# Optimization experiments

Hardware: AMD Instinct MI355X
Metric: run time of the kernel (lower is better)

Reference implementation:

```python
import jax, jax.numpy as jnp
import numpy as np

N = 50000   # nodes
E = 800000  # edges
G = 256     # graphs in batch
NF, EF, H, L = 16, 8, 128, 4
EPS = 1e-5


def setup_inputs() -> dict:
    key = jax.random.key(0)
    ks = jax.random.split(key, 20)
    s = 0.05
    return {
        "x": jax.random.normal(ks[0], (N, NF), jnp.float32),
        "edge_index": jax.random.randint(ks[1], (2, E), 0, N, dtype=jnp.int32),
        "edge_attr": jax.random.uniform(ks[2], (E, EF), jnp.float32),
        "batch": jnp.sort(jax.random.randint(ks[3], (N,), 0, G, dtype=jnp.int32)),
        "W_emb": jax.random.normal(ks[4], (NF, H), jnp.float32) * s,
        "b_emb": jnp.zeros((H,), jnp.float32),
        "Wf": jax.random.normal(ks[5], (L, 2 * H + EF, H), jnp.float32) * s,
        "bf": jnp.zeros((L, H), jnp.float32),
        "Ws": jax.random.normal(ks[6], (L, 2 * H + EF, H), jnp.float32) * s,
        "bs": jnp.zeros((L, H), jnp.float32),
        "gamma": jnp.ones((L, H), jnp.float32),
        "beta": jnp.zeros((L, H), jnp.float32),
        "W1": jax.random.normal(ks[7], (H, 64), jnp.float32) * s,
        "b1": jnp.zeros((64,), jnp.float32),
        "W2": jax.random.normal(ks[8], (64, 32), jnp.float32) * s,
        "b2": jnp.zeros((32,), jnp.float32),
        "W_out": jax.random.normal(ks[9], (32, 1), jnp.float32) * s,
        "b_out": jnp.zeros((1,), jnp.float32),
    }


def reference(x, edge_index, edge_attr, batch, W_emb, b_emb, Wf, bf, Ws, bs,
              gamma, beta, W1, b1, W2, b2, W_out, b_out):
    src, dst = edge_index[0], edge_index[1]  # message j->i: x_j=h[src], x_i=h[dst]
    h = jax.nn.relu(x @ W_emb + b_emb)       # [N, H]
    for l in range(L):
        # CGConv: z_ij = [x_i, x_j, e_ij]; gated message; sum-aggregate; +x residual
        z = jnp.concatenate([h[dst], h[src], edge_attr], axis=-1)  # [E, 2H+EF]
        m = jax.nn.sigmoid(z @ Wf[l] + bf[l]) * jax.nn.softplus(z @ Ws[l] + bs[l])
        agg = jax.ops.segment_sum(m, dst, num_segments=N)
        x_new = agg + h
        # BatchNorm1d (training-mode batch statistics, biased var)
        mu = x_new.mean(axis=0)
        var = x_new.var(axis=0)
        x_new = gamma[l] * (x_new - mu) * jax.lax.rsqrt(var + EPS) + beta[l]
        x_new = jax.nn.relu(x_new)
        h = h + x_new
    # global mean pool over graphs
    cnt = jax.ops.segment_sum(jnp.ones((N,), h.dtype), batch, num_segments=G)
    pooled = jax.ops.segment_sum(h, batch, num_segments=G) / jnp.maximum(cnt, 1.0)[:, None]
    g = jax.nn.relu(pooled @ W1 + b1)
    g = jax.nn.relu(g @ W2 + b2)
    return (g @ W_out + b_out).squeeze(-1)  # [G]
```

## Files before the change

### kernel.cpp

```cpp
#include <hip/hip_runtime.h>
#include <hip/hip_bf16.h>

#define H 128
#define EFD 8
#define NLAYER 4
#define ZDIM (2*H+EFD)

typedef float f32x2 __attribute__((ext_vector_type(2)));
typedef float f32x4 __attribute__((ext_vector_type(4)));
typedef short s16x8 __attribute__((ext_vector_type(8)));
typedef _Float16 f16x4 __attribute__((ext_vector_type(4)));

#define PKFMA_LO(acc, a, b) asm("v_pk_fma_f32 %0, %1, %2, %0 op_sel:[0,0,0] op_sel_hi:[0,1,1]" : "+v"(acc) : "v"(a), "v"(b))
#define PKFMA_HI(acc, a, b) asm("v_pk_fma_f32 %0, %1, %2, %0 op_sel:[1,0,0] op_sel_hi:[1,1,1]" : "+v"(acc) : "v"(a), "v"(b))
#define PKFMA_LO_INIT(dst, a, b, c) asm("v_pk_fma_f32 %0, %1, %2, %3 op_sel:[0,0,0] op_sel_hi:[0,1,1]" : "=v"(dst) : "v"(a), "v"(b), "v"(c))

#define L2E 1.44269504088896340736f
#define LN2 0.69314718055994530942f

__device__ __forceinline__ unsigned short f2bf(float x){
    unsigned u = __float_as_uint(x);
    return (unsigned short)((u + 0x7FFFu + ((u>>16)&1u)) >> 16);
}

__global__ void embed_kernel(const float* __restrict__ x, const float* __restrict__ We,
                             const float* __restrict__ be, float* __restrict__ h, int N){
    int idx = blockIdx.x*blockDim.x + threadIdx.x;
    if (idx >= N*H) return;
    int n = idx >> 7, f = idx & 127;
    float a = be[f];
    #pragma unroll
    for (int k=0;k<16;k++) a = fmaf(x[n*16+k], We[k*H+f], a);
    h[idx] = fmaxf(a, 0.f);
}

__global__ void hist_kernel(const int* __restrict__ dstI, int* __restrict__ counts, int E){
    int e = blockIdx.x*blockDim.x + threadIdx.x;
    if (e < E) atomicAdd(&counts[dstI[e]], 1);
}

__global__ __launch_bounds__(1024) void scan1(const int* __restrict__ counts, int* __restrict__ incl,
                                              int* __restrict__ bsums, int N){
    __shared__ int lds[1024];
    int t = threadIdx.x;
    int i = blockIdx.x*1024 + t;
    int v = (i < N) ? counts[i] : 0;
    lds[t] = v;
    __syncthreads();
    for (int off=1; off<1024; off<<=1){
        int add = (t>=off) ? lds[t-off] : 0;
        __syncthreads();
        lds[t] += add;
        __syncthreads();
    }
    if (i < N) incl[i] = lds[t];
    if (t == 1023) bsums[blockIdx.x] = lds[1023];
}

__global__ void scan2(int* bsums, int nb){
    if (threadIdx.x == 0){
        int run = 0;
        for (int b=0;b<nb;b++){ int v = bsums[b]; bsums[b] = run; run += v; }
    }
}

__global__ __launch_bounds__(1024) void scan3(const int* incl, const int* __restrict__ counts,
                                              const int* __restrict__ bsums, int* __restrict__ rowptr,
                                              int* cursor, int N, int E){
    int i = blockIdx.x*1024 + threadIdx.x;
    if (i >= N) return;
    int ex = incl[i] - counts[i] + bsums[blockIdx.x];
    rowptr[i] = ex;
    cursor[i] = ex;
    if (i == N-1) rowptr[N] = E;
}

__global__ void scatter_kernel(const int* __restrict__ srcI, const int* __restrict__ dstI,
                               const float* __restrict__ eattr, int* __restrict__ cursor,
                               int* __restrict__ src_s, float* __restrict__ ea_s, int E){
    int e = blockIdx.x*blockDim.x + threadIdx.x;
    if (e >= E) return;
    int d = dstI[e];
    int pos = atomicAdd(&cursor[d], 1);
    src_s[pos] = srcI[e];
    const float4* s4 = (const float4*)(eattr + (size_t)e*EFD);
    float4* o4 = (float4*)(ea_s + (size_t)pos*EFD);
    o4[0] = s4[0]; o4[1] = s4[1];
}

__global__ __launch_bounds__(256) void wpack_kernel(const float* __restrict__ Wf, const float* __restrict__ Ws,
        s16x8* __restrict__ bhi, s16x8* __restrict__ blo){
    int idx = blockIdx.x*256 + threadIdx.x;
    int l = idx & 63, ct = (idx>>6)&7, ks = (idx>>9)&3, w = (idx>>11)&3, layer = idx>>13;
    int cp = w*128 + ct*16 + (l&15);
    int k0 = ks*32 + ((l>>4)<<3);
    const float* WfL = Wf + (size_t)layer*ZDIM*H;
    const float* WsL = Ws + (size_t)layer*ZDIM*H;
    int colIn = cp & 127;
    int sel = cp >> 7;
    const float* Wm = (sel & 1) ? WsL : WfL;
    int krow = (sel >> 1) ? H : 0;
    s16x8 vh, vl;
    #pragma unroll
    for (int e=0;e<8;e++){
        float v = Wm[(size_t)(krow + k0 + e)*H + colIn];
        unsigned short hb = f2bf(v);
        float rem = v - __uint_as_float(((unsigned)hb)<<16);
        vh[e] = (short)hb;
        vl[e] = (short)f2bf(rem);
    }
    bhi[idx] = vh;
    blo[idx] = vl;
}

__global__ __launch_bounds__(256, 2) void table_mfma(
        float* __restrict__ h, const float* __restrict__ xn, const float* __restrict__ scsh,
        const s16x8* __restrict__ bhi, const s16x8* __restrict__ blo,
        const float* __restrict__ bf_l, const float* __restrict__ bs_l,
        float* __restrict__ TD, _Float16* __restrict__ TS16, int N, int layer){
    __shared__ __align__(16) short amat[2][32*136];
    const int t = threadIdx.x;
    const int n0 = blockIdx.x*32;
    {
        const int row = t >> 3, kb = (t & 7)*16;
        const int gn = n0 + row;
        const bool valid = gn < N;
        float* hr = h + (size_t)gn*H + kb;
        float vv[16];
        if (scsh){
            float sc[16], sh[16];
            #pragma unroll
            for (int q=0;q<16;q+=4){
                *(float4*)&sc[q] = *(const float4*)(scsh + kb + q);
                *(float4*)&sh[q] = *(const float4*)(scsh + H + kb + q);
            }
            const float* xr = xn + (size_t)gn*H + kb;
            #pragma unroll
            for (int q=0;q<16;q+=4){
                float4 xv = valid ? *(const float4*)(xr + q) : make_float4(0.f,0.f,0.f,0.f);
                float4 hv = valid ? *(const float4*)(hr + q) : make_float4(0.f,0.f,0.f,0.f);
                vv[q]   = hv.x + fmaxf(fmaf(xv.x, sc[q],   sh[q]),   0.f);
                vv[q+1] = hv.y + fmaxf(fmaf(xv.y, sc[q+1], sh[q+1]), 0.f);
                vv[q+2] = hv.z + fmaxf(fmaf(xv.z, sc[q+2], sh[q+2]), 0.f);
                vv[q+3] = hv.w + fmaxf(fmaf(xv.w, sc[q+3], sh[q+3]), 0.f);
            }
            if (valid){
                #pragma unroll
                for (int q=0;q<16;q+=4){
                    float4 o; o.x=vv[q]; o.y=vv[q+1]; o.z=vv[q+2]; o.w=vv[q+3];
                    *(float4*)(hr + q) = o;
                }
            }
        } else {
            #pragma unroll
            for (int q=0;q<16;q+=4){
                float4 hv = valid ? *(const float4*)(hr + q) : make_float4(0.f,0.f,0.f,0.f);
                vv[q]=hv.x; vv[q+1]=hv.y; vv[q+2]=hv.z; vv[q+3]=hv.w;
            }
        }
        s16x8 hv2[2], lv2[2];
        #pragma unroll
        for (int q=0;q<16;q++){
            unsigned short hb = f2bf(vv[q]);
            float rem = vv[q] - __uint_as_float(((unsigned)hb)<<16);
            hv2[q>>3][q&7] = (short)hb;
            lv2[q>>3][q&7] = (short)f2bf(rem);
        }
        short* dh = &amat[0][row*136 + kb];
        short* dl = &amat[1][row*136 + kb];
        *(s16x8*)dh = hv2[0]; *(s16x8*)(dh+8) = hv2[1];
        *(s16x8*)dl = lv2[0]; *(s16x8*)(dl+8) = lv2[1];
    }
    __syncthreads();
    const int lane = t & 63, w = t >> 6;
    const int rbase = lane & 15, kg = lane >> 4;
    f32x4 acc[2][8];
    #pragma unroll
    for (int rt=0;rt<2;rt++)
        #pragma unroll
        for (int ct=0;ct<8;ct++){ acc[rt][ct][0]=0.f; acc[rt][ct][1]=0.f; acc[rt][ct][2]=0.f; acc[rt][ct][3]=0.f; }
    const size_t bbase = ((size_t)layer*4 + w)*2048;
    #pragma unroll
    for (int ks=0;ks<4;ks++){
        s16x8 bh[8], bl[8];
        #pragma unroll
        for (int ct=0;ct<8;ct++){
            bh[ct] = bhi[bbase + ks*512 + ct*64 + lane];
            bl[ct] = blo[bbase + ks*512 + ct*64 + lane];
        }
        s16x8 ah[2], al[2];
        #pragma unroll
        for (int rt=0;rt<2;rt++){
            const int ao = (rbase + 16*rt)*136 + ks*32 + kg*8;
            ah[rt] = *(const s16x8*)&amat[0][ao];
            al[rt] = *(const s16x8*)&amat[1][ao];
        }
        #pragma unroll
        for (int ct=0;ct<8;ct++)
            #pragma unroll
            for (int rt=0;rt<2;rt++){
                acc[rt][ct] = __builtin_amdgcn_mfma_f32_16x16x32_bf16(ah[rt], bh[ct], acc[rt][ct], 0, 0, 0);
                acc[rt][ct] = __builtin_amdgcn_mfma_f32_16x16x32_bf16(ah[rt], bl[ct], acc[rt][ct], 0, 0, 0);
                acc[rt][ct] = __builtin_amdgcn_mfma_f32_16x16x32_bf16(al[rt], bh[ct], acc[rt][ct], 0, 0, 0);
            }
    }
    if (w < 2){
        float* outb = TD;
        const int colbase = (w & 1)*128;
        const float* bias = (w == 0) ? bf_l : bs_l;
        #pragma unroll
        for (int ct=0;ct<8;ct++){
            const int c_local = ct*16 + rbase;
            const float bv = bias[c_local]*L2E;
            #pragma unroll
            for (int rt=0;rt<2;rt++){
                const int nrow0 = n0 + 16*rt + kg*4;
                #pragma unroll
                for (int r=0;r<4;r++){
                    const int nd = nrow0 + r;
                    if (nd < N) outb[(size_t)nd*256 + colbase + c_local] = fmaf(acc[rt][ct][r], L2E, bv);
                }
            }
        }
    } else {
        const int slot = (w & 1) << 1;
        #pragma unroll
        for (int ct=0;ct<8;ct++){
            const int c_local = ct*16 + rbase;
            const int off = (c_local >> 1)*4 + slot + (c_local & 1);
            #pragma unroll
            for (int rt=0;rt<2;rt++){
                const int nrow0 = n0 + 16*rt + kg*4;
                #pragma unroll
                for (int r=0;r<4;r++){
                    const int nd = nrow0 + r;
                    if (nd < N) TS16[(size_t)nd*256 + off] = (_Float16)(acc[rt][ct][r]*L2E);
                }
            }
        }
    }
}

__global__ __launch_bounds__(256, 4) void agg_kernel(
        const float* __restrict__ TD, const _Float16* __restrict__ TS16,
        const int* __restrict__ rowptr, const int* __restrict__ src_s, const float* __restrict__ ea_s,
        const float* __restrict__ Wf_l, const float* __restrict__ Ws_l,
        const float* __restrict__ h, float* __restrict__ xn, int N){
    __shared__ float wE[2048];
    const int t = threadIdx.x;
    {
        const float4* a = (const float4*)(Wf_l + 2*H*H);
        const float4* b = (const float4*)(Ws_l + 2*H*H);
        float4 va = a[t], vb = b[t];
        va.x*=L2E; va.y*=L2E; va.z*=L2E; va.w*=L2E;
        vb.x*=L2E; vb.y*=L2E; vb.z*=L2E; vb.w*=L2E;
        ((float4*)wE)[t] = va;
        ((float4*)wE)[256 + t] = vb;
    }
    __syncthreads();
    const int k = t & 63;
    const int i = blockIdx.x*4 + (t >> 6);
    if (i >= N) return;
    f32x2 wef2[8], wes2[8];
    #pragma unroll
    for (int r=0;r<8;r++){
        wef2[r] = *(const f32x2*)&wE[r*128 + 2*k];
        wes2[r] = *(const f32x2*)&wE[1024 + r*128 + 2*k];
    }
    #pragma unroll
    for (int r=0;r<8;r++) asm volatile("" : "+v"(wef2[r]), "+v"(wes2[r]));
    const f32x2* td = (const f32x2*)(TD + ((size_t)i << 8));
    f32x2 fd2 = td[k], sd2 = td[64+k];
    f32x2 acc = {0.f, 0.f};
    const int e0 = __builtin_amdgcn_readfirstlane(rowptr[i]);
    const int e1 = __builtin_amdgcn_readfirstlane(rowptr[i+1]);
    const int myoff = 4*k;
    for (int ebase = e0; ebase < e1; ebase += 64){
        const int ecnt = min(64, e1 - ebase);
        const int ids = (k < ecnt) ? src_s[ebase + k] : 0;
        int j = __builtin_amdgcn_readlane(ids, 0);
        f16x4 tv = *(const f16x4*)(TS16 + (((size_t)(unsigned)j) << 8) + myoff);
        for (int q = 0; q < ecnt; ++q){
            const int jn = __builtin_amdgcn_readlane(ids, (q+1 < ecnt) ? (q+1) : q);
            f16x4 tvn = *(const f16x4*)(TS16 + (((size_t)(unsigned)jn) << 8) + myoff);
            const float* ep = ea_s + (size_t)(ebase + q)*EFD;
            f32x4 eaA = *(const f32x4*)(ep);
            f32x4 eaB = *(const f32x4*)(ep + 4);
            f32x2 ea0 = __builtin_shufflevector(eaA, eaA, 0, 1);
            f32x2 ea1 = __builtin_shufflevector(eaA, eaA, 2, 3);
            f32x2 ea2 = __builtin_shufflevector(eaB, eaB, 0, 1);
            f32x2 ea3 = __builtin_shufflevector(eaB, eaB, 2, 3);
            f32x2 ef, es;
            PKFMA_LO_INIT(ef, ea0, wef2[0], fd2);
            PKFMA_HI(ef, ea0, wef2[1]);
            PKFMA_LO(ef, ea1, wef2[2]); PKFMA_HI(ef, ea1, wef2[3]);
            PKFMA_LO(ef, ea2, wef2[4]); PKFMA_HI(ef, ea2, wef2[5]);
            PKFMA_LO(ef, ea3, wef2[6]); PKFMA_HI(ef, ea3, wef2[7]);
            PKFMA_LO_INIT(es, ea0, wes2[0], sd2);
            PKFMA_HI(es, ea0, wes2[1]);
            PKFMA_LO(es, ea1, wes2[2]); PKFMA_HI(es, ea1, wes2[3]);
            PKFMA_LO(es, ea2, wes2[4]); PKFMA_HI(es, ea2, wes2[5]);
            PKFMA_LO(es, ea3, wes2[6]); PKFMA_HI(es, ea3, wes2[7]);
            f32x2 g = ef, p = es;
            g.x += (float)tv[0]; g.y += (float)tv[1];
            p.x += (float)tv[2]; p.y += (float)tv[3];
            float sx = __builtin_amdgcn_rcpf(1.0f + __builtin_amdgcn_exp2f(-g.x));
            float sy = __builtin_amdgcn_rcpf(1.0f + __builtin_amdgcn_exp2f(-g.y));
            float tx = fmaxf(p.x, 0.f) + __builtin_amdgcn_logf(1.0f + __builtin_amdgcn_exp2f(-fabsf(p.x)));
            float ty = fmaxf(p.y, 0.f) + __builtin_amdgcn_logf(1.0f + __builtin_amdgcn_exp2f(-fabsf(p.y)));
            acc.x = fmaf(sx*tx, LN2, acc.x);
            acc.y = fmaf(sy*ty, LN2, acc.y);
            tv = tvn;
        }
    }
    f32x2 hv = *(const f32x2*)(h + ((size_t)i << 7) + 2*k);
    f32x2 o = acc + hv;
    *(f32x2*)(xn + ((size_t)i << 7) + 2*k) = o;
}

__global__ __launch_bounds__(256) void stats_kernel(const float* __restrict__ xn, double* __restrict__ sums, int N){
    __shared__ double l1[128], l2[128];
    const int f = threadIdx.x & 127;
    const int half = threadIdx.x >> 7;
    const int nb = gridDim.x;
    const int per = (N + nb - 1)/nb;
    const int r0 = blockIdx.x*per;
    const int r1 = min(N, r0+per);
    double s = 0.0, s2 = 0.0;
    for (int r=r0+half; r<r1; r+=2){
        float v = xn[(size_t)r*H + f];
        s += v; s2 += (double)v*(double)v;
    }
    if (half == 1){ l1[f] = s; l2[f] = s2; }
    __syncthreads();
    if (half == 0){
        s += l1[f]; s2 += l2[f];
        atomicAdd(&sums[f], s);
        atomicAdd(&sums[H+f], s2);
    }
}

__global__ void finalize_bn(double* __restrict__ sums, const float* __restrict__ gamma_l,
                            const float* __restrict__ beta_l, float* __restrict__ scsh, int N){
    int f = threadIdx.x;
    if (f >= H) return;
    double mu = sums[f]/(double)N;
    double var = sums[H+f]/(double)N - mu*mu;
    if (var < 0.0) var = 0.0;
    float sc = (float)((double)gamma_l[f] / sqrt(var + 1e-5));
    scsh[f]   = sc;
    scsh[H+f] = (float)((double)beta_l[f] - mu*(double)sc);
    sums[f] = 0.0;
    sums[H+f] = 0.0;
}

__global__ __launch_bounds__(128) void pool_mlp_kernel(const float* __restrict__ h, const float* __restrict__ xn,
        const float* __restrict__ scsh, const int* __restrict__ batch,
        const float* __restrict__ W1, const float* __restrict__ b1,
        const float* __restrict__ W2, const float* __restrict__ b2,
        const float* __restrict__ Wo, const float* __restrict__ bo,
        float* __restrict__ out, int N){
    __shared__ float row[128];
    __shared__ float g1[64];
    __shared__ float g2[32];
    const int g = blockIdx.x;
    const int t = threadIdx.x;
    int lo = 0, hi = N;
    while (lo < hi){ int m = (lo+hi)>>1; if (batch[m] < g) lo = m+1; else hi = m; }
    const int s0 = lo;
    hi = N;
    while (lo < hi){ int m = (lo+hi)>>1; if (batch[m] < g+1) lo = m+1; else hi = m; }
    const int s1 = lo;
    const float sc = scsh[t], sh = scsh[H+t];
    float acc = 0.f;
    for (int r = s0; r < s1; ++r){
        float hv = h[(size_t)r*H + t];
        float xv = xn[(size_t)r*H + t];
        acc += hv + fmaxf(fmaf(xv, sc, sh), 0.f);
    }
    const float inv = 1.0f/fmaxf((float)(s1-s0), 1.0f);
    row[t] = acc*inv;
    __syncthreads();
    if (t < 64){
        float a = b1[t];
        #pragma unroll 4
        for (int i2=0;i2<128;i2++) a = fmaf(row[i2], W1[i2*64+t], a);
        g1[t] = fmaxf(a, 0.f);
    }
    __syncthreads();
    if (t < 32){
        float b = b2[t];
        #pragma unroll 4
        for (int i2=0;i2<64;i2++) b = fmaf(g1[i2], W2[i2*32+t], b);
        g2[t] = fmaxf(b, 0.f);
    }
    __syncthreads();
    if (t < 64){
        float p = (t < 32) ? g2[t]*Wo[t] : 0.f;
        for (int off=32; off>0; off>>=1) p += __shfl_down(p, off);
        if (t == 0) out[g] = p + bo[0];
    }
}

extern "C" void kernel_launch(void* const* d_in, const int* in_sizes, int n_in,
                              void* d_out, int out_size, void* d_ws, size_t ws_size,
                              hipStream_t stream){
    const float* x     = (const float*)d_in[0];
    const int*   eidx  = (const int*)d_in[1];
    const float* eattr = (const float*)d_in[2];
    const int*   batch = (const int*)d_in[3];
    const float* W_emb = (const float*)d_in[4];
    const float* b_emb = (const float*)d_in[5];
    const float* Wf    = (const float*)d_in[6];
    const float* bf    = (const float*)d_in[7];
    const float* Wsm   = (const float*)d_in[8];
    const float* bs    = (const float*)d_in[9];
    const float* gamma = (const float*)d_in[10];
    const float* beta  = (const float*)d_in[11];
    const float* W1    = (const float*)d_in[12];
    const float* b1    = (const float*)d_in[13];
    const float* W2    = (const float*)d_in[14];
    const float* b2    = (const float*)d_in[15];
    const float* Wo    = (const float*)d_in[16];
    const float* bo    = (const float*)d_in[17];
    float* out = (float*)d_out;

    const int N = in_sizes[0]/16;
    const int E = in_sizes[1]/2;
    const int G = out_size;

    const int* srcI = eidx;
    const int* dstI = eidx + E;

    char* p = (char*)d_ws;
    auto alloc = [&](size_t bytes)->char*{ char* r = p; p += (bytes + 255) & ~255ull; return r; };
    float*     h      = (float*)     alloc((size_t)N*H*4);
    float*     xn     = (float*)     alloc((size_t)N*H*4);
    float*     TD     = (float*)     alloc((size_t)N*2*H*4);
    _Float16*  TS16   = (_Float16*)  alloc((size_t)N*2*H*2);
    float*     ea_s   = (float*)     alloc((size_t)E*EFD*4);
    int*       src_s  = (int*)       alloc((size_t)E*4);
    int*       rowptr = (int*)       alloc((size_t)(N+1)*4);
    int*       cursor = (int*)       alloc((size_t)N*4);
    int*       counts = (int*)       alloc((size_t)N*4);
    int*       bsums  = (int*)       alloc(256*4);
    double*    sums   = (double*)    alloc(2*H*8);
    float*     scsh   = (float*)     alloc(2*H*4);
    s16x8*     bhi    = (s16x8*)     alloc((size_t)NLAYER*8192*16);
    s16x8*     blo    = (s16x8*)     alloc((size_t)NLAYER*8192*16);

    const int thr = 256;
    hipMemsetAsync(counts, 0, (size_t)N*4, stream);
    hipMemsetAsync(sums, 0, 2*H*8, stream);
    embed_kernel<<<(N*H + thr-1)/thr, thr, 0, stream>>>(x, W_emb, b_emb, h, N);
    hist_kernel<<<(E + thr-1)/thr, thr, 0, stream>>>(dstI, counts, E);
    int nb = (N + 1023)/1024;
    scan1<<<nb, 1024, 0, stream>>>(counts, cursor, bsums, N);
    scan2<<<1, 64, 0, stream>>>(bsums, nb);
    scan3<<<nb, 1024, 0, stream>>>(cursor, counts, bsums, rowptr, cursor, N, E);
    scatter_kernel<<<(E + thr-1)/thr, thr, 0, stream>>>(srcI, dstI, eattr, cursor, src_s, ea_s, E);
    wpack_kernel<<<128, 256, 0, stream>>>(Wf, Wsm, bhi, blo);

    for (int l=0;l<NLAYER;l++){
        const float* Wf_l = Wf  + (size_t)l*ZDIM*H;
        const float* Ws_l = Wsm + (size_t)l*ZDIM*H;
        table_mfma<<<(N+31)/32, 256, 0, stream>>>(h, xn, (l==0)?nullptr:scsh, bhi, blo,
                                                  bf + l*H, bs + l*H, TD, TS16, N, l);
        agg_kernel<<<(N+3)/4, 256, 0, stream>>>(TD, TS16, rowptr, src_s, ea_s, Wf_l, Ws_l, h, xn, N);
        stats_kernel<<<256, 256, 0, stream>>>(xn, sums, N);
        finalize_bn<<<1, 128, 0, stream>>>(sums, gamma + l*H, beta + l*H, scsh, N);
    }

    pool_mlp_kernel<<<G, 128, 0, stream>>>(h, xn, scsh, batch, W1, b1, W2, b2, Wo, bo, out, N);
}
```

Before: 939.1 us.

## Make table MFMA kernel persistent with register-resident weights; simplify agg edge loop

The table kernel becomes persistent: 256 blocks of 512 threads each loop over 32-row node tiles. Each of the 8 waves holds its slice of the split-bf16 weight fragments in registers for the whole run, instead of reloading them from global memory for every tile. The aggregation kernel drops its 64-edge batched src-id load with readlane and reads each next source index per edge via readfirstlane. The aim is to cut repeated weight traffic, at the cost of higher register pressure and an extra barrier per tile.

```diff
diff --git a/kernel.cpp b/kernel.cpp
--- a/kernel.cpp
+++ b/kernel.cpp
@@ -113,131 +113,145 @@
     blo[idx] = vl;
 }
 
-__global__ __launch_bounds__(256, 2) void table_mfma(
+__global__ __launch_bounds__(512, 2) void table_mfma(
         float* __restrict__ h, const float* __restrict__ xn, const float* __restrict__ scsh,
         const s16x8* __restrict__ bhi, const s16x8* __restrict__ blo,
         const float* __restrict__ bf_l, const float* __restrict__ bs_l,
-        float* __restrict__ TD, _Float16* __restrict__ TS16, int N, int layer){
+        float* __restrict__ TD, _Float16* __restrict__ TS16, int N, int layer, int ntiles){
     __shared__ __align__(16) short amat[2][32*136];
     const int t = threadIdx.x;
-    const int n0 = blockIdx.x*32;
+    const int lane = t & 63, W = t >> 6;
+    const int ow = W >> 1, ctbase = (W & 1)*4;
+    const int rbase = lane & 15, kg = lane >> 4;
+
+    s16x8 Bh[4][4], Bl[4][4];
     {
-        const int row = t >> 3, kb = (t & 7)*16;
-        const int gn = n0 + row;
-        const bool valid = gn < N;
-        float* hr = h + (size_t)gn*H + kb;
-        float vv[16];
-        if (scsh){
-            float sc[16], sh[16];
-            #pragma unroll
-            for (int q=0;q<16;q+=4){
-                *(float4*)&sc[q] = *(const float4*)(scsh + kb + q);
-                *(float4*)&sh[q] = *(const float4*)(scsh + H + kb + q);
+        const size_t bbase = ((size_t)layer*4 + ow)*2048;
+        #pragma unroll
+        for (int ks=0;ks<4;ks++)
+            #pragma unroll
+            for (int c=0;c<4;c++){
+                Bh[ks][c] = bhi[bbase + ks*512 + (ctbase+c)*64 + lane];
+                Bl[ks][c] = blo[bbase + ks*512 + (ctbase+c)*64 + lane];
             }
-            const float* xr = xn + (size_t)gn*H + kb;
-            #pragma unroll
-            for (int q=0;q<16;q+=4){
-                float4 xv = valid ? *(const float4*)(xr + q) : make_float4(0.f,0.f,0.f,0.f);
-                float4 hv = valid ? *(const float4*)(hr + q) : make_float4(0.f,0.f,0.f,0.f);
-                vv[q]   = hv.x + fmaxf(fmaf(xv.x, sc[q],   sh[q]),   0.f);
-                vv[q+1] = hv.y + fmaxf(fmaf(xv.y, sc[q+1], sh[q+1]), 0.f);
-                vv[q+2] = hv.z + fmaxf(fmaf(xv.z, sc[q+2], sh[q+2]), 0.f);
-                vv[q+3] = hv.w + fmaxf(fmaf(xv.w, sc[q+3], sh[q+3]), 0.f);
+        #pragma unroll
+        for (int ks=0;ks<4;ks++)
+            #pragma unroll
+            for (int c=0;c<4;c++) asm volatile("" : "+v"(Bh[ks][c]), "+v"(Bl[ks][c]));
+    }
+    int c_local[4], off16[4];
+    float bv[4];
+    #pragma unroll
+    for (int c=0;c<4;c++){
+        c_local[c] = (ctbase+c)*16 + rbase;
+        off16[c] = (c_local[c] >> 1)*4 + ((ow & 1) << 1) + (c_local[c] & 1);
+        bv[c] = (ow == 0) ? bf_l[c_local[c]]*L2E : (ow == 1) ? bs_l[c_local[c]]*L2E : 0.f;
+    }
+    const int srow = t >> 4;
+    const int kb = (t & 15)*8;
+    float sc8[8], sh8[8];
+    if (scsh){
+        #pragma unroll
+        for (int q=0;q<8;q+=4){
+            *(float4*)&sc8[q] = *(const float4*)(scsh + kb + q);
+            *(float4*)&sh8[q] = *(const float4*)(scsh + H + kb + q);
+        }
+    }
+
+    for (int tile = blockIdx.x; tile < ntiles; tile += gridDim.x){
+        const int n0 = tile*32;
+        {
+            const int gn = n0 + srow;
+            const bool valid = gn < N;
+            float* hr = h + (size_t)gn*H + kb;
+            float vv[8];
+            if (scsh){
+                const float* xr = xn + (size_t)gn*H + kb;
+                #pragma unroll
+                for (int q=0;q<8;q+=4){
+                    float4 xv = valid ? *(const float4*)(xr + q) : make_float4(0.f,0.f,0.f,0.f);
+                    float4 hv = valid ? *(const float4*)(hr + q) : make_float4(0.f,0.f,0.f,0.f);
+                    vv[q]   = hv.x + fmaxf(fmaf(xv.x, sc8[q],   sh8[q]),   0.f);
+                    vv[q+1] = hv.y + fmaxf(fmaf(xv.y, sc8[q+1], sh8[q+1]), 0.f);
+                    vv[q+2] = hv.z + fmaxf(fmaf(xv.z, sc8[q+2], sh8[q+2]), 0.f);
+                    vv[q+3] = hv.w + fmaxf(fmaf(xv.w, sc8[q+3], sh8[q+3]), 0.f);
+                }
+                if (valid){
+                    #pragma unroll
+                    for (int q=0;q<8;q+=4){
+                        float4 o; o.x=vv[q]; o.y=vv[q+1]; o.z=vv[q+2]; o.w=vv[q+3];
+                        *(float4*)(hr + q) = o;
+                    }
+                }
+            } else {
+                #pragma unroll
+                for (int q=0;q<8;q+=4){
+                    float4 hv = valid ? *(const float4*)(hr + q) : make_float4(0.f,0.f,0.f,0.f);
+                    vv[q]=hv.x; vv[q+1]=hv.y; vv[q+2]=hv.z; vv[q+3]=hv.w;
+                }
             }
-            if (valid){
+            s16x8 hv2, lv2;
+            #pragma unroll
+            for (int q=0;q<8;q++){
+                unsigned short hb = f2bf(vv[q]);
+                float rem = vv[q] - __uint_as_float(((unsigned)hb)<<16);
+                hv2[q] = (short)hb;
+                lv2[q] = (short)f2bf(rem);
+            }
+            *(s16x8*)&amat[0][srow*136 + kb] = hv2;
+            *(s16x8*)&amat[1][srow*136 + kb] = lv2;
+        }
+        __syncthreads();
+        f32x4 acc[2][4];
+        #pragma unroll
+        for (int rt=0;rt<2;rt++)
+            #pragma unroll
+            for (int c=0;c<4;c++){ acc[rt][c][0]=0.f; acc[rt][c][1]=0.f; acc[rt][c][2]=0.f; acc[rt][c][3]=0.f; }
+        #pragma unroll
+        for (int ks=0;ks<4;ks++){
+            s16x8 ah[2], al[2];
+            #pragma unroll
+            for (int rt=0;rt<2;rt++){
+                const int ao = (rbase + 16*rt)*136 + ks*32 + kg*8;
+                ah[rt] = *(const s16x8*)&amat[0][ao];
+                al[rt] = *(const s16x8*)&amat[1][ao];
+            }
+            #pragma unroll
+            for (int c=0;c<4;c++)
                 #pragma unroll
-                for (int q=0;q<16;q+=4){
-                    float4 o; o.x=vv[q]; o.y=vv[q+1]; o.z=vv[q+2]; o.w=vv[q+3];
-                    *(float4*)(hr + q) = o;
-                }
-            }
+                for (int rt=0;rt<2;rt++){
+                    acc[rt][c] = __builtin_amdgcn_mfma_f32_16x16x32_bf16(ah[rt], Bh[ks][c], acc[rt][c], 0, 0, 0);
+                    acc[rt][c] = __builtin_amdgcn_mfma_f32_16x16x32_bf16(ah[rt], Bl[ks][c], acc[rt][c], 0, 0, 0);
+                    acc[rt][c] = __builtin_amdgcn_mfma_f32_16x16x32_bf16(al[rt], Bh[ks][c], acc[rt][c], 0, 0, 0);
+                }
+        }
+        if (ow < 2){
+            const int colbase = (ow & 1)*128;
+            #pragma unroll
+            for (int c=0;c<4;c++)
+                #pragma unroll
+                for (int rt=0;rt<2;rt++){
+                    const int nrow0 = n0 + 16*rt + kg*4;
+                    #pragma unroll
+                    for (int r=0;r<4;r++){
+                        const int nd = nrow0 + r;
+                        if (nd < N) TD[(size_t)nd*256 + colbase + c_local[c]] = fmaf(acc[rt][c][r], L2E, bv[c]);
+                    }
+                }
         } else {
             #pragma unroll
-            for (int q=0;q<16;q+=4){
-                float4 hv = valid ? *(const float4*)(hr + q) : make_float4(0.f,0.f,0.f,0.f);
-                vv[q]=hv.x; vv[q+1]=hv.y; vv[q+2]=hv.z; vv[q+3]=hv.w;
-            }
+            for (int c=0;c<4;c++)
+                #pragma unroll
+                for (int rt=0;rt<2;rt++){
+                    const int nrow0 = n0 + 16*rt + kg*4;
+                    #pragma unroll
+                    for (int r=0;r<4;r++){
+                        const int nd = nrow0 + r;
+                        if (nd < N) TS16[(size_t)nd*256 + off16[c]] = (_Float16)(acc[rt][c][r]*L2E);
+                    }
+                }
         }
-        s16x8 hv2[2], lv2[2];
-        #pragma unroll
-        for (int q=0;q<16;q++){
-            unsigned short hb = f2bf(vv[q]);
-            float rem = vv[q] - __uint_as_float(((unsigned)hb)<<16);
-            hv2[q>>3][q&7] = (short)hb;
-            lv2[q>>3][q&7] = (short)f2bf(rem);
-        }
-        short* dh = &amat[0][row*136 + kb];
-        short* dl = &amat[1][row*136 + kb];
-        *(s16x8*)dh = hv2[0]; *(s16x8*)(dh+8) = hv2[1];
-        *(s16x8*)dl = lv2[0]; *(s16x8*)(dl+8) = lv2[1];
-    }
-    __syncthreads();
-    const int lane = t & 63, w = t >> 6;
-    const int rbase = lane & 15, kg = lane >> 4;
-    f32x4 acc[2][8];
-    #pragma unroll
-    for (int rt=0;rt<2;rt++)
-        #pragma unroll
-        for (int ct=0;ct<8;ct++){ acc[rt][ct][0]=0.f; acc[rt][ct][1]=0.f; acc[rt][ct][2]=0.f; acc[rt][ct][3]=0.f; }
-    const size_t bbase = ((size_t)layer*4 + w)*2048;
-    #pragma unroll
-    for (int ks=0;ks<4;ks++){
-        s16x8 bh[8], bl[8];
-        #pragma unroll
-        for (int ct=0;ct<8;ct++){
-            bh[ct] = bhi[bbase + ks*512 + ct*64 + lane];
-            bl[ct] = blo[bbase + ks*512 + ct*64 + lane];
-        }
-        s16x8 ah[2], al[2];
-        #pragma unroll
-        for (int rt=0;rt<2;rt++){
-            const int ao = (rbase + 16*rt)*136 + ks*32 + kg*8;
-            ah[rt] = *(const s16x8*)&amat[0][ao];
-            al[rt] = *(const s16x8*)&amat[1][ao];
-        }
-        #pragma unroll
-        for (int ct=0;ct<8;ct++)
-            #pragma unroll
-            for (int rt=0;rt<2;rt++){
-                acc[rt][ct] = __builtin_amdgcn_mfma_f32_16x16x32_bf16(ah[rt], bh[ct], acc[rt][ct], 0, 0, 0);
-                acc[rt][ct] = __builtin_amdgcn_mfma_f32_16x16x32_bf16(ah[rt], bl[ct], acc[rt][ct], 0, 0, 0);
-                acc[rt][ct] = __builtin_amdgcn_mfma_f32_16x16x32_bf16(al[rt], bh[ct], acc[rt][ct], 0, 0, 0);
-            }
-    }
-    if (w < 2){
-        float* outb = TD;
-        const int colbase = (w & 1)*128;
-        const float* bias = (w == 0) ? bf_l : bs_l;
-        #pragma unroll
-        for (int ct=0;ct<8;ct++){
-            const int c_local = ct*16 + rbase;
-            const float bv = bias[c_local]*L2E;
-            #pragma unroll
-            for (int rt=0;rt<2;rt++){
-                const int nrow0 = n0 + 16*rt + kg*4;
-                #pragma unroll
-                for (int r=0;r<4;r++){
-                    const int nd = nrow0 + r;
-                    if (nd < N) outb[(size_t)nd*256 + colbase + c_local] = fmaf(acc[rt][ct][r], L2E, bv);
-                }
-            }
-        }
-    } else {
-        const int slot = (w & 1) << 1;
-        #pragma unroll
-        for (int ct=0;ct<8;ct++){
-            const int c_local = ct*16 + rbase;
-            const int off = (c_local >> 1)*4 + slot + (c_local & 1);
-            #pragma unroll
-            for (int rt=0;rt<2;rt++){
-                const int nrow0 = n0 + 16*rt + kg*4;
-                #pragma unroll
-                for (int r=0;r<4;r++){
-                    const int nd = nrow0 + r;
-                    if (nd < N) TS16[(size_t)nd*256 + off] = (_Float16)(acc[rt][ct][r]*L2E);
-                }
-            }
-        }
+        __syncthreads();
     }
 }
 
@@ -275,43 +289,40 @@
     const int e0 = __builtin_amdgcn_readfirstlane(rowptr[i]);
     const int e1 = __builtin_amdgcn_readfirstlane(rowptr[i+1]);
     const int myoff = 4*k;
-    for (int ebase = e0; ebase < e1; ebase += 64){
-        const int ecnt = min(64, e1 - ebase);
-        const int ids = (k < ecnt) ? src_s[ebase + k] : 0;
-        int j = __builtin_amdgcn_readlane(ids, 0);
-        f16x4 tv = *(const f16x4*)(TS16 + (((size_t)(unsigned)j) << 8) + myoff);
-        for (int q = 0; q < ecnt; ++q){
-            const int jn = __builtin_amdgcn_readlane(ids, (q+1 < ecnt) ? (q+1) : q);
-            f16x4 tvn = *(const f16x4*)(TS16 + (((size_t)(unsigned)jn) << 8) + myoff);
-            const float* ep = ea_s + (size_t)(ebase + q)*EFD;
-            f32x4 eaA = *(const f32x4*)(ep);
-            f32x4 eaB = *(const f32x4*)(ep + 4);
-            f32x2 ea0 = __builtin_shufflevector(eaA, eaA, 0, 1);
-            f32x2 ea1 = __builtin_shufflevector(eaA, eaA, 2, 3);
-            f32x2 ea2 = __builtin_shufflevector(eaB, eaB, 0, 1);
-            f32x2 ea3 = __builtin_shufflevector(eaB, eaB, 2, 3);
-            f32x2 ef, es;
-            PKFMA_LO_INIT(ef, ea0, wef2[0], fd2);
-            PKFMA_HI(ef, ea0, wef2[1]);
-            PKFMA_LO(ef, ea1, wef2[2]); PKFMA_HI(ef, ea1, wef2[3]);
-            PKFMA_LO(ef, ea2, wef2[4]); PKFMA_HI(ef, ea2, wef2[5]);
-            PKFMA_LO(ef, ea3, wef2[6]); PKFMA_HI(ef, ea3, wef2[7]);
-            PKFMA_LO_INIT(es, ea0, wes2[0], sd2);
-            PKFMA_HI(es, ea0, wes2[1]);
-            PKFMA_LO(es, ea1, wes2[2]); PKFMA_HI(es, ea1, wes2[3]);
-            PKFMA_LO(es, ea2, wes2[4]); PKFMA_HI(es, ea2, wes2[5]);
-            PKFMA_LO(es, ea3, wes2[6]); PKFMA_HI(es, ea3, wes2[7]);
-            f32x2 g = ef, p = es;
-            g.x += (float)tv[0]; g.y += (float)tv[1];
-            p.x += (float)tv[2]; p.y += (float)tv[3];
-            float sx = __builtin_amdgcn_rcpf(1.0f + __builtin_amdgcn_exp2f(-g.x));
-            float sy = __builtin_amdgcn_rcpf(1.0f + __builtin_amdgcn_exp2f(-g.y));
-            float tx = fmaxf(p.x, 0.f) + __builtin_amdgcn_logf(1.0f + __builtin_amdgcn_exp2f(-fabsf(p.x)));
-            float ty = fmaxf(p.y, 0.f) + __builtin_amdgcn_logf(1.0f + __builtin_amdgcn_exp2f(-fabsf(p.y)));
-            acc.x = fmaf(sx*tx, LN2, acc.x);
-            acc.y = fmaf(sy*ty, LN2, acc.y);
-            tv = tvn;
-        }
+    int j = (e0 < e1) ? __builtin_amdgcn_readfirstlane(src_s[e0]) : 0;
+    f16x4 tv = *(const f16x4*)(TS16 + (((size_t)(unsigned)j) << 8) + myoff);
+    for (int e = e0; e < e1; ++e){
+        const int en = (e+1 < e1) ? (e+1) : e;
+        const int jn = __builtin_amdgcn_readfirstlane(src_s[en]);
+        f16x4 tvn = *(const f16x4*)(TS16 + (((size_t)(unsigned)jn) << 8) + myoff);
+        const float* ep = ea_s + (size_t)e*EFD;
+        f32x4 eaA = *(const f32x4*)(ep);
+        f32x4 eaB = *(const f32x4*)(ep + 4);
+        f32x2 ea0 = __builtin_shufflevector(eaA, eaA, 0, 1);
+        f32x2 ea1 = __builtin_shufflevector(eaA, eaA, 2, 3);
+        f32x2 ea2 = __builtin_shufflevector(eaB, eaB, 0, 1);
+        f32x2 ea3 = __builtin_shufflevector(eaB, eaB, 2, 3);
+        f32x2 ef, es;
+        PKFMA_LO_INIT(ef, ea0, wef2[0], fd2);
+        PKFMA_HI(ef, ea0, wef2[1]);
+        PKFMA_LO(ef, ea1, wef2[2]); PKFMA_HI(ef, ea1, wef2[3]);
+        PKFMA_LO(ef, ea2, wef2[4]); PKFMA_HI(ef, ea2, wef2[5]);
+        PKFMA_LO(ef, ea3, wef2[6]); PKFMA_HI(ef, ea3, wef2[7]);
+        PKFMA_LO_INIT(es, ea0, wes2[0], sd2);
+        PKFMA_HI(es, ea0, wes2[1]);
+        PKFMA_LO(es, ea1, wes2[2]); PKFMA_HI(es, ea1, wes2[3]);
+        PKFMA_LO(es, ea2, wes2[4]); PKFMA_HI(es, ea2, wes2[5]);
+        PKFMA_LO(es, ea3, wes2[6]); PKFMA_HI(es, ea3, wes2[7]);
+        f32x2 g = ef, p = es;
+        g.x += (float)tv[0]; g.y += (float)tv[1];
+        p.x += (float)tv[2]; p.y += (float)tv[3];
+        float sx = __builtin_amdgcn_rcpf(1.0f + __builtin_amdgcn_exp2f(-g.x));
+        float sy = __builtin_amdgcn_rcpf(1.0f + __builtin_amdgcn_exp2f(-g.y));
+        float tx = fmaxf(p.x, 0.f) + __builtin_amdgcn_logf(1.0f + __builtin_amdgcn_exp2f(-fabsf(p.x)));
+        float ty = fmaxf(p.y, 0.f) + __builtin_amdgcn_logf(1.0f + __builtin_amdgcn_exp2f(-fabsf(p.y)));
+        acc.x = fmaf(sx*tx, LN2, acc.x);
+        acc.y = fmaf(sy*ty, LN2, acc.y);
+        tv = tvn; j = jn;
     }
     f32x2 hv = *(const f32x2*)(h + ((size_t)i << 7) + 2*k);
     f32x2 o = acc + hv;
@@ -461,11 +472,12 @@
     scatter_kernel<<<(E + thr-1)/thr, thr, 0, stream>>>(srcI, dstI, eattr, cursor, src_s, ea_s, E);
     wpack_kernel<<<128, 256, 0, stream>>>(Wf, Wsm, bhi, blo);
 
+    const int ntiles = (N + 31)/32;
     for (int l=0;l<NLAYER;l++){
         const float* Wf_l = Wf  + (size_t)l*ZDIM*H;
         const float* Ws_l = Wsm + (size_t)l*ZDIM*H;
-        table_mfma<<<(N+31)/32, 256, 0, stream>>>(h, xn, (l==0)?nullptr:scsh, bhi, blo,
-                                                  bf + l*H, bs + l*H, TD, TS16, N, l);
+        table_mfma<<<256, 512, 0, stream>>>(h, xn, (l==0)?nullptr:scsh, bhi, blo,
+                                            bf + l*H, bs + l*H, TD, TS16, N, l, ntiles);
         agg_kernel<<<(N+3)/4, 256, 0, stream>>>(TD, TS16, rowptr, src_s, ea_s, Wf_l, Ws_l, h, xn, N);
         stats_kernel<<<256, 256, 0, stream>>>(xn, sums, N);
         finalize_bn<<<1, 128, 0, stream>>>(sums, gamma + l*H, beta + l*H, scsh, N);
```

Result: faster. 866.6 us (-7.7%).
